# Performance work log

Measured on AMD Instinct MI355X. Metric: run time of the kernel, lower is better.

## Reference

```python
import jax, jax.numpy as jnp
import numpy as np
from math import sqrt

B, L, S, H, E, D = 2, 2048, 2048, 8, 64, 64


def setup_inputs() -> dict:
    key = jax.random.key(0)
    kq, kk, kv, kb = jax.random.split(key, 4)
    queries = jax.random.normal(kq, (B, L, H, E), dtype=jnp.float32)
    keys = jax.random.normal(kk, (B, S, H, E), dtype=jnp.float32)
    values = jax.random.normal(kv, (B, S, H, D), dtype=jnp.float32)
    # TriangularCausalMask: True above the diagonal (positions to mask)
    causal = jnp.triu(jnp.ones((L, S), dtype=bool), k=1)
    attn_mask = jnp.broadcast_to(causal[None, None], (B, 1, L, S))
    attn_bias = jax.random.normal(kb, (B, L, S, H), dtype=jnp.float32) * 0.1
    return {"queries": queries, "keys": keys, "values": values,
            "attn_mask": attn_mask, "attn_bias": attn_bias}


def reference(queries, keys, values, attn_mask, attn_bias):
    scale = 1.0 / sqrt(E)
    # scores: [B, H, L, S]
    scores = jnp.einsum('blhe,bshe->bhls', queries, keys)
    scores = jnp.where(attn_mask, -jnp.inf, scores)
    bias = jnp.transpose(attn_bias, (0, 3, 1, 2))  # [B,H,L,S]
    A = jax.nn.softmax(scores * scale + bias, axis=-1)  # dropout = identity (eval)
    V = jnp.einsum('bhls,bshd->blhd', A, values)
    return V
```

## Files before the change

### kernel.cpp

```cpp
#include <hip/hip_runtime.h>
#include <stdint.h>

#define Bb 2
#define Ll 2048
#define Ss 2048
#define Hh 8
#define Ee 64
#define Dd 64

#define LOG2E 1.4426950408889634f
#define QSCALE (0.125f * LOG2E)
#define NEG_BIG (-1e30f)
#define QT_ELEMS 2097152

typedef short bf16x8 __attribute__((ext_vector_type(8)));
typedef short bf16x4 __attribute__((ext_vector_type(4)));
typedef float f32x4  __attribute__((ext_vector_type(4)));

__device__ __forceinline__ short f2bf(float f) {
  uint32_t u = __float_as_uint(f);
  u += 0x7fffu + ((u >> 16) & 1u);
  return (short)(u >> 16);
}
__device__ __forceinline__ float bf2f(short s) {
  return __uint_as_float(((uint32_t)(unsigned short)s) << 16);
}
__device__ __forceinline__ f32x4 mfma_pv(bf16x4 a, bf16x4 b, f32x4 c) {
#if __has_builtin(__builtin_amdgcn_mfma_f32_16x16x16_bf16)
  return __builtin_amdgcn_mfma_f32_16x16x16_bf16(a, b, c, 0, 0, 0);
#else
  return __builtin_amdgcn_mfma_f32_16x16x16bf16_1k(a, b, c, 0, 0, 0);
#endif
}

#define BLOCK_SYNC() do {                                   \
    asm volatile("s_waitcnt lgkmcnt(0)" ::: "memory");      \
    __builtin_amdgcn_s_barrier();                           \
    asm volatile("" ::: "memory");                          \
  } while (0)

__global__ __launch_bounds__(256)
void prep_qkv(const float* __restrict__ Q, const float* __restrict__ K,
              const float* __restrict__ V, short* __restrict__ Qt,
              short* __restrict__ Kt, short* __restrict__ Vt)
{
  const int blk = blockIdx.x;
  const int tid = threadIdx.x;
  if (blk < 1024) {
    const int c = tid & 15;
    #pragma unroll
    for (int pass = 0; pass < 4; ++pass) {
      const int rowg = blk * 64 + pass * 16 + (tid >> 4);
      const int tensor = rowg >> 15;
      const int r2 = rowg & 32767;
      const float* src = (tensor ? K : Q) + (size_t)r2 * 64 + c * 4;
      const float4 v = *(const float4*)(src);
      const int b = r2 >> 14, l = (r2 >> 3) & 2047, hh = r2 & 7;
      const float sc = tensor ? 1.0f : QSCALE;
      bf16x4 o;
      o[0] = f2bf(v.x * sc); o[1] = f2bf(v.y * sc);
      o[2] = f2bf(v.z * sc); o[3] = f2bf(v.w * sc);
      short* dst = (tensor ? Kt : Qt) + ((size_t)((b * 8 + hh) * 2048 + l)) * 64 + c * 4;
      *reinterpret_cast<bf16x4*>(dst) = o;
    }
  } else {
    const int vb = blk - 1024;
    const int plane = vb >> 5;
    const int b = plane >> 3, hh = plane & 7;
    const int sc = (vb & 31) * 64;
    const int w = tid >> 6, d = tid & 63;
    const int sbase = sc + w * 16;
    const float* src = V + (((size_t)b * Ss + sbase) * Hh + hh) * Dd + d;
    float vals[16];
    #pragma unroll
    for (int i = 0; i < 16; ++i) vals[i] = src[(size_t)i * (Hh * Dd)];
    bf16x8 o0, o1;
    #pragma unroll
    for (int i = 0; i < 8; ++i) { o0[i] = f2bf(vals[i]); o1[i] = f2bf(vals[i + 8]); }
    short* dst = Vt + ((size_t)(plane * 64 + d)) * 2048 + sbase;
    *reinterpret_cast<bf16x8*>(dst)     = o0;
    *reinterpret_cast<bf16x8*>(dst + 8) = o1;
  }
}

__global__ __launch_bounds__(256, 1)
void fattn6(const short* __restrict__ Qt, const short* __restrict__ Kt,
            const short* __restrict__ Vt, const float* __restrict__ Bias,
            float* __restrict__ Out)
{
  __shared__ short Vs[2][4][64][72];
  __shared__ short Bs[2][4][4][16][16];

  const int tid  = threadIdx.x;
  const int wv   = tid >> 6;
  const int lane = tid & 63;
  const int g    = lane >> 4;
  const int n    = lane & 15;

  const int rid    = blockIdx.x;
  const int xcd    = rid & 7;
  const int b      = xcd >> 2;
  const int hhalf  = (xcd >> 1) & 1;
  const int z      = xcd & 1;
  const int pairid = (rid >> 3) * 2 + z;
  const int h      = hhalf * 4 + wv;
  const int p      = b * 8 + h;

  const int sl = tid >> 4;
  const int sq = tid & 15;
  const int srcb = (lane & 48) | ((lane >> 2) & 12);

  const short* vglob = Vt + ((size_t)((b * 8 + hhalf * 4) * 64) + (tid >> 3)) * 2048
                          + (tid & 7) * 8;
  short* vlds = &Vs[0][0][tid >> 3][(tid & 7) * 8];

#define ISSUE_V(VN, soff) do {                                              \
    _Pragma("unroll")                                                       \
    for (int k_ = 0; k_ < 8; ++k_)                                          \
      VN[k_] = *reinterpret_cast<const bf16x8*>(                            \
          vglob + (size_t)(k_ >> 1) * (64 * 2048)                           \
                + (size_t)(k_ & 1) * (32 * 2048) + (soff));                 \
  } while (0)

#define WRITE_V(buf, VN) do {                                               \
    _Pragma("unroll")                                                       \
    for (int k_ = 0; k_ < 8; ++k_)                                          \
      *reinterpret_cast<bf16x8*>(vlds + (size_t)(buf) * (4 * 64 * 72)       \
          + (k_ >> 1) * (64 * 72) + (k_ & 1) * (32 * 72)) = VN[k_];         \
  } while (0)

  for (int job = 0; job < 2; ++job) {
    const int lg = job ? pairid : (127 - pairid);
    const int l0 = lg * 16;
    const int ntiles = (lg >> 2) + 1;
    const int lq = l0 + n;

    const short* qp = Qt + ((size_t)(p * 2048 + l0 + n)) * 64 + g * 8;
    const bf16x8 qf0 = *reinterpret_cast<const bf16x8*>(qp);
    const bf16x8 qf1 = *reinterpret_cast<const bf16x8*>(qp + 32);

    const short* kbase = Kt + ((size_t)(p * 2048 + n)) * 64 + g * 8;
    const float* gb = Bias + (((size_t)(b * Ll + l0 + sl)) * Ss + sq) * Hh + hhalf * 4;

    f32x4 acc[4];
    #pragma unroll
    for (int dt = 0; dt < 4; ++dt) { f32x4 zz = {0.f,0.f,0.f,0.f}; acc[dt] = zz; }
    float m = NEG_BIG, lsum = 0.f;

    bf16x8 kA[4][2], kB[4][2];
    float4 gB0, gB1, gB2, gB3;

#define ISSUE_K(KN, soff) do {                                              \
      const short* kp_ = kbase + (size_t)(soff) * 64;                       \
      _Pragma("unroll")                                                     \
      for (int st_ = 0; st_ < 4; ++st_) {                                   \
        KN[st_][0] = *reinterpret_cast<const bf16x8*>(kp_ + st_ * 16 * 64); \
        KN[st_][1] = *reinterpret_cast<const bf16x8*>(kp_ + st_ * 16 * 64 + 32); \
      }                                                                     \
    } while (0)

#define ISSUE_BIAS(G0, G1, G2, G3, soff) do {                               \
      const float* gp_ = gb + (size_t)(soff) * Hh;                          \
      G0 = *(const float4*)(gp_);                                           \
      G1 = *(const float4*)(gp_ + (size_t)16 * Hh);                         \
      G2 = *(const float4*)(gp_ + (size_t)32 * Hh);                         \
      G3 = *(const float4*)(gp_ + (size_t)48 * Hh);                         \
    } while (0)

#define WRITE_BIAS(buf, G0, G1, G2, G3) do {                                \
      short* w0_ = &Bs[buf][0][0][sl][sq];                                  \
      short* w1_ = &Bs[buf][0][1][sl][sq];                                  \
      short* w2_ = &Bs[buf][0][2][sl][sq];                                  \
      short* w3_ = &Bs[buf][0][3][sl][sq];                                  \
      w0_[0]=f2bf(G0.x*LOG2E); w0_[1024]=f2bf(G0.y*LOG2E); w0_[2048]=f2bf(G0.z*LOG2E); w0_[3072]=f2bf(G0.w*LOG2E); \
      w1_[0]=f2bf(G1.x*LOG2E); w1_[1024]=f2bf(G1.y*LOG2E); w1_[2048]=f2bf(G1.z*LOG2E); w1_[3072]=f2bf(G1.w*LOG2E); \
      w2_[0]=f2bf(G2.x*LOG2E); w2_[1024]=f2bf(G2.y*LOG2E); w2_[2048]=f2bf(G2.z*LOG2E); w2_[3072]=f2bf(G2.w*LOG2E); \
      w3_[0]=f2bf(G3.x*LOG2E); w3_[1024]=f2bf(G3.y*LOG2E); w3_[2048]=f2bf(G3.z*LOG2E); w3_[3072]=f2bf(G3.w*LOG2E); \
    } while (0)

    {
      float4 a0, a1, a2, a3;
      ISSUE_BIAS(a0, a1, a2, a3, 0);
      ISSUE_BIAS(gB0, gB1, gB2, gB3, 64);
      ISSUE_K(kA, 0);
      bf16x8 v0[8];
      ISSUE_V(v0, 0);
      WRITE_BIAS(0, a0, a1, a2, a3);
      WRITE_V(0, v0);
    }
    BLOCK_SYNC();

#define TILE(KC, KN, t) do {                                                \
      const int s0_ = (t) * 64;                                             \
      const int cb_ = (t) & 1, nb_ = cb_ ^ 1;                               \
      const bool more1_ = ((t) + 1 < ntiles);                               \
      const bool more2_ = ((t) + 2 < ntiles);                               \
                 \
      if (more1_) ISSUE_K(KN, s0_ + 64);                                    \
      bf16x8 vN_[8];                                                        \
      if (more1_) ISSUE_V(vN_, s0_ + 64);                                   \
                                                    \
      f32x4 sacc_[4];                                                       \
      _Pragma("unroll")                                                     \
      for (int st_ = 0; st_ < 4; ++st_) {                                   \
        const bf16x4 bb_ = *reinterpret_cast<const bf16x4*>(&Bs[cb_][wv][st_][n][4 * g]); \
        f32x4 zz_ = {0.f, 0.f, 0.f, 0.f};                                   \
        f32x4 sv_ = __builtin_amdgcn_mfma_f32_16x16x32_bf16(KC[st_][0], qf0, zz_, 0, 0, 0); \
        sv_ = __builtin_amdgcn_mfma_f32_16x16x32_bf16(KC[st_][1], qf1, sv_, 0, 0, 0); \
        const int sb_ = s0_ + st_ * 16 + 4 * g;                             \
        _Pragma("unroll")                                                   \
        for (int r_ = 0; r_ < 4; ++r_)                                      \
          sacc_[st_][r_] = (sb_ + r_ <= lq) ? (sv_[r_] + bf2f(bb_[r_])) : NEG_BIG; \
      }                                                                     \
                                            \
      float tm_ = NEG_BIG;                                                  \
      _Pragma("unroll")                                                     \
      for (int st_ = 0; st_ < 4; ++st_)                                     \
        _Pragma("unroll")                                                   \
        for (int r_ = 0; r_ < 4; ++r_) tm_ = fmaxf(tm_, sacc_[st_][r_]);    \
      tm_ = fmaxf(tm_, __shfl_xor(tm_, 16));                                \
      tm_ = fmaxf(tm_, __shfl_xor(tm_, 32));                                \
      if (__any(tm_ - m > 8.f)) {                                           \
        const float mn_ = fmaxf(m, tm_);                                    \
        const float corr_ = exp2f(m - mn_);                                 \
        m = mn_; lsum *= corr_;                                             \
        const float c0_ = __shfl(corr_, srcb);                              \
        const float c1_ = __shfl(corr_, srcb + 1);                          \
        const float c2_ = __shfl(corr_, srcb + 2);                          \
        const float c3_ = __shfl(corr_, srcb + 3);                          \
        _Pragma("unroll")                                                   \
        for (int dt_ = 0; dt_ < 4; ++dt_) {                                 \
          acc[dt_][0] *= c0_; acc[dt_][1] *= c1_;                           \
          acc[dt_][2] *= c2_; acc[dt_][3] *= c3_;                           \
        }                                                                   \
      }                                                                     \
      bf16x4 pa_[4];                                                        \
      float ps_ = 0.f;                                                      \
      _Pragma("unroll")                                                     \
      for (int st_ = 0; st_ < 4; ++st_) {                                   \
        _Pragma("unroll")                                                   \
        for (int r_ = 0; r_ < 4; ++r_) {                                    \
          const float pe_ = exp2f(sacc_[st_][r_] - m);                      \
          ps_ += pe_;                                                       \
          pa_[st_][r_] = f2bf(pe_);                                         \
        }                                                                   \
      }                                                                     \
      ps_ += __shfl_xor(ps_, 16);                                           \
      ps_ += __shfl_xor(ps_, 32);                                           \
      lsum += ps_;                                                          \
                   \
      _Pragma("unroll")                                                     \
      for (int st_ = 0; st_ < 4; ++st_) {                                   \
        _Pragma("unroll")                                                   \
        for (int dt_ = 0; dt_ < 4; ++dt_) {                                 \
          const bf16x4 vb_ = *reinterpret_cast<const bf16x4*>(              \
              &Vs[cb_][wv][dt_ * 16 + n][st_ * 16 + 4 * g]);                \
          acc[dt_] = mfma_pv(pa_[st_], vb_, acc[dt_]);                      \
        }                                                                   \
      }                                                                     \
                                  \
      if (more1_) {                                                         \
        WRITE_V(nb_, vN_);                                                  \
        WRITE_BIAS(nb_, gB0, gB1, gB2, gB3);                                \
      }                                                                     \
      if (more2_) ISSUE_BIAS(gB0, gB1, gB2, gB3, s0_ + 128);                \
      BLOCK_SYNC();                                                         \
    } while (0)

    int t = 0;
    for (;;) {
      TILE(kA, kB, t); if (++t == ntiles) break;
      TILE(kB, kA, t); if (++t == ntiles) break;
    }

    const float i0 = 1.0f / __shfl(lsum, srcb);
    const float i1 = 1.0f / __shfl(lsum, srcb + 1);
    const float i2 = 1.0f / __shfl(lsum, srcb + 2);
    const float i3 = 1.0f / __shfl(lsum, srcb + 3);
    float* ob = Out + ((size_t)((b * Ll + l0 + 4 * g) * Hh + h)) * Dd + n;
    #pragma unroll
    for (int dt = 0; dt < 4; ++dt) {
      ob[0 * Hh * Dd + dt * 16] = acc[dt][0] * i0;
      ob[1 * Hh * Dd + dt * 16] = acc[dt][1] * i1;
      ob[2 * Hh * Dd + dt * 16] = acc[dt][2] * i2;
      ob[3 * Hh * Dd + dt * 16] = acc[dt][3] * i3;
    }

#undef TILE
#undef WRITE_BIAS
#undef ISSUE_BIAS
#undef ISSUE_K
  }
#undef WRITE_V
#undef ISSUE_V
}

extern "C" void kernel_launch(void* const* d_in, const int* in_sizes, int n_in,
                              void* d_out, int out_size, void* d_ws, size_t ws_size,
                              hipStream_t stream) {
  const float* Q    = (const float*)d_in[0];
  const float* K    = (const float*)d_in[1];
  const float* V    = (const float*)d_in[2];
  const float* Bias = (const float*)d_in[4];
  float* Out = (float*)d_out;

  short* wsp = (short*)d_ws;
  short* Qt = wsp;
  short* Kt = wsp + QT_ELEMS;
  short* Vt = wsp + 2 * (size_t)QT_ELEMS;

  prep_qkv<<<dim3(1536), dim3(256), 0, stream>>>(Q, K, V, Qt, Kt, Vt);
  fattn6<<<dim3(256), dim3(256), 0, stream>>>(Qt, Kt, Vt, Bias, Out);
}
```

Before: 94.14 us.

## Split each key tile across two wave groups with split-softmax merge

Doubles the block to 512 threads so two groups of four waves each process half of every 64-key tile, with per-group running max and sum. At the end the two partial accumulators are merged through shared memory using max and exp rescaling before the output is written. The goal is more waves in flight per CU to hide latency on this memory- and latency-bound causal attention. In exchange it adds extra shared memory, extra block barriers, and a final merge step. The masked score value also changes to a more negative sentinel.

After: 83.03 us. 11.8% less time.

```diff
diff --git a/kernel.cpp b/kernel.cpp
--- a/kernel.cpp
+++ b/kernel.cpp
@@ -10,7 +10,8 @@
 
 #define LOG2E 1.4426950408889634f
 #define QSCALE (0.125f * LOG2E)
-#define NEG_BIG (-1e30f)
+#define NEG_BIG  (-1e30f)
+#define NEG_MASK (-3.0e38f)
 #define QT_ELEMS 2097152
 
 typedef short bf16x8 __attribute__((ext_vector_type(8)));
@@ -83,16 +84,20 @@
   }
 }
 
-__global__ __launch_bounds__(256, 1)
-void fattn6(const short* __restrict__ Qt, const short* __restrict__ Kt,
+__global__ __launch_bounds__(512, 2)
+void fattn8(const short* __restrict__ Qt, const short* __restrict__ Kt,
             const short* __restrict__ Vt, const float* __restrict__ Bias,
             float* __restrict__ Out)
 {
   __shared__ short Vs[2][4][64][72];
   __shared__ short Bs[2][4][4][16][16];
+  __shared__ float Os[4][16][68];
+  __shared__ float mb[2][4][16];
+  __shared__ float lb[2][4][16];
 
   const int tid  = threadIdx.x;
-  const int wv   = tid >> 6;
+  const int sh   = tid >> 8;
+  const int wv   = (tid >> 6) & 3;
   const int lane = tid & 63;
   const int g    = lane >> 4;
   const int n    = lane & 15;
@@ -105,28 +110,27 @@
   const int pairid = (rid >> 3) * 2 + z;
   const int h      = hhalf * 4 + wv;
   const int p      = b * 8 + h;
-
-  const int sl = tid >> 4;
-  const int sq = tid & 15;
+  const int p0     = b * 8 + hhalf * 4;
+
+  const int vch = tid & 7;
+  const int vr  = (tid >> 3) & 63;
+  const short* vglob = Vt + ((size_t)(p0 * 64 + vr)) * 2048 + vch * 8;
+
+  const int sl  = tid >> 5;
+  const int sq2 = tid & 31;
   const int srcb = (lane & 48) | ((lane >> 2) & 12);
-
-  const short* vglob = Vt + ((size_t)((b * 8 + hhalf * 4) * 64) + (tid >> 3)) * 2048
-                          + (tid & 7) * 8;
-  short* vlds = &Vs[0][0][tid >> 3][(tid & 7) * 8];
 
 #define ISSUE_V(VN, soff) do {                                              \
     _Pragma("unroll")                                                       \
-    for (int k_ = 0; k_ < 8; ++k_)                                          \
+    for (int k_ = 0; k_ < 4; ++k_)                                          \
       VN[k_] = *reinterpret_cast<const bf16x8*>(                            \
-          vglob + (size_t)(k_ >> 1) * (64 * 2048)                           \
-                + (size_t)(k_ & 1) * (32 * 2048) + (soff));                 \
+          vglob + (size_t)k_ * (64 * 2048) + (soff));                       \
   } while (0)
 
 #define WRITE_V(buf, VN) do {                                               \
     _Pragma("unroll")                                                       \
-    for (int k_ = 0; k_ < 8; ++k_)                                          \
-      *reinterpret_cast<bf16x8*>(vlds + (size_t)(buf) * (4 * 64 * 72)       \
-          + (k_ >> 1) * (64 * 72) + (k_ & 1) * (32 * 72)) = VN[k_];         \
+    for (int k_ = 0; k_ < 4; ++k_)                                          \
+      *reinterpret_cast<bf16x8*>(&Vs[buf][k_][vr][vch * 8]) = VN[k_];       \
   } while (0)
 
   for (int job = 0; job < 2; ++job) {
@@ -139,53 +143,52 @@
     const bf16x8 qf0 = *reinterpret_cast<const bf16x8*>(qp);
     const bf16x8 qf1 = *reinterpret_cast<const bf16x8*>(qp + 32);
 
-    const short* kbase = Kt + ((size_t)(p * 2048 + n)) * 64 + g * 8;
-    const float* gb = Bias + (((size_t)(b * Ll + l0 + sl)) * Ss + sq) * Hh + hhalf * 4;
+    const short* kbase = Kt + ((size_t)(p * 2048 + sh * 32 + n)) * 64 + g * 8;
+    const float* gb = Bias + (((size_t)(b * Ll + l0 + sl)) * Ss + sq2) * Hh + hhalf * 4;
 
     f32x4 acc[4];
     #pragma unroll
     for (int dt = 0; dt < 4; ++dt) { f32x4 zz = {0.f,0.f,0.f,0.f}; acc[dt] = zz; }
     float m = NEG_BIG, lsum = 0.f;
 
-    bf16x8 kA[4][2], kB[4][2];
-    float4 gB0, gB1, gB2, gB3;
+    bf16x8 kA[2][2], kB[2][2];
+    float4 gB0, gB1;
 
 #define ISSUE_K(KN, soff) do {                                              \
       const short* kp_ = kbase + (size_t)(soff) * 64;                       \
       _Pragma("unroll")                                                     \
-      for (int st_ = 0; st_ < 4; ++st_) {                                   \
+      for (int st_ = 0; st_ < 2; ++st_) {                                   \
         KN[st_][0] = *reinterpret_cast<const bf16x8*>(kp_ + st_ * 16 * 64); \
         KN[st_][1] = *reinterpret_cast<const bf16x8*>(kp_ + st_ * 16 * 64 + 32); \
       }                                                                     \
     } while (0)
 
-#define ISSUE_BIAS(G0, G1, G2, G3, soff) do {                               \
+#define ISSUE_BIAS(G0, G1, soff) do {                                       \
       const float* gp_ = gb + (size_t)(soff) * Hh;                          \
       G0 = *(const float4*)(gp_);                                           \
-      G1 = *(const float4*)(gp_ + (size_t)16 * Hh);                         \
-      G2 = *(const float4*)(gp_ + (size_t)32 * Hh);                         \
-      G3 = *(const float4*)(gp_ + (size_t)48 * Hh);                         \
+      G1 = *(const float4*)(gp_ + (size_t)32 * Hh);                         \
     } while (0)
 
-#define WRITE_BIAS(buf, G0, G1, G2, G3) do {                                \
-      short* w0_ = &Bs[buf][0][0][sl][sq];                                  \
-      short* w1_ = &Bs[buf][0][1][sl][sq];                                  \
-      short* w2_ = &Bs[buf][0][2][sl][sq];                                  \
-      short* w3_ = &Bs[buf][0][3][sl][sq];                                  \
-      w0_[0]=f2bf(G0.x*LOG2E); w0_[1024]=f2bf(G0.y*LOG2E); w0_[2048]=f2bf(G0.z*LOG2E); w0_[3072]=f2bf(G0.w*LOG2E); \
-      w1_[0]=f2bf(G1.x*LOG2E); w1_[1024]=f2bf(G1.y*LOG2E); w1_[2048]=f2bf(G1.z*LOG2E); w1_[3072]=f2bf(G1.w*LOG2E); \
-      w2_[0]=f2bf(G2.x*LOG2E); w2_[1024]=f2bf(G2.y*LOG2E); w2_[2048]=f2bf(G2.z*LOG2E); w2_[3072]=f2bf(G2.w*LOG2E); \
-      w3_[0]=f2bf(G3.x*LOG2E); w3_[1024]=f2bf(G3.y*LOG2E); w3_[2048]=f2bf(G3.z*LOG2E); w3_[3072]=f2bf(G3.w*LOG2E); \
+#define WRITE_BIAS(buf, G0, G1) do {                                        \
+      const int st0_ = sq2 >> 4, s16_ = sq2 & 15;                           \
+      Bs[buf][0][st0_][sl][s16_]     = f2bf(G0.x * LOG2E);                  \
+      Bs[buf][1][st0_][sl][s16_]     = f2bf(G0.y * LOG2E);                  \
+      Bs[buf][2][st0_][sl][s16_]     = f2bf(G0.z * LOG2E);                  \
+      Bs[buf][3][st0_][sl][s16_]     = f2bf(G0.w * LOG2E);                  \
+      Bs[buf][0][st0_ + 2][sl][s16_] = f2bf(G1.x * LOG2E);                  \
+      Bs[buf][1][st0_ + 2][sl][s16_] = f2bf(G1.y * LOG2E);                  \
+      Bs[buf][2][st0_ + 2][sl][s16_] = f2bf(G1.z * LOG2E);                  \
+      Bs[buf][3][st0_ + 2][sl][s16_] = f2bf(G1.w * LOG2E);                  \
     } while (0)
 
     {
-      float4 a0, a1, a2, a3;
-      ISSUE_BIAS(a0, a1, a2, a3, 0);
-      ISSUE_BIAS(gB0, gB1, gB2, gB3, 64);
+      float4 a0, a1;
+      ISSUE_BIAS(a0, a1, 0);
+      ISSUE_BIAS(gB0, gB1, 64);
       ISSUE_K(kA, 0);
-      bf16x8 v0[8];
+      bf16x8 v0[4];
       ISSUE_V(v0, 0);
-      WRITE_BIAS(0, a0, a1, a2, a3);
+      WRITE_BIAS(0, a0, a1);
       WRITE_V(0, v0);
     }
     BLOCK_SYNC();
@@ -195,29 +198,29 @@
       const int cb_ = (t) & 1, nb_ = cb_ ^ 1;                               \
       const bool more1_ = ((t) + 1 < ntiles);                               \
       const bool more2_ = ((t) + 2 < ntiles);                               \
-                 \
       if (more1_) ISSUE_K(KN, s0_ + 64);                                    \
-      bf16x8 vN_[8];                                                        \
+      bf16x8 vN_[4];                                                        \
       if (more1_) ISSUE_V(vN_, s0_ + 64);                                   \
-                                                    \
-      f32x4 sacc_[4];                                                       \
-      _Pragma("unroll")                                                     \
-      for (int st_ = 0; st_ < 4; ++st_) {                                   \
-        const bf16x4 bb_ = *reinterpret_cast<const bf16x4*>(&Bs[cb_][wv][st_][n][4 * g]); \
+                            \
+      f32x4 sacc_[2];                                                       \
+      _Pragma("unroll")                                                     \
+      for (int stl_ = 0; stl_ < 2; ++stl_) {                                \
+        const int stg_ = 2 * sh + stl_;                                     \
+        const bf16x4 bb_ = *reinterpret_cast<const bf16x4*>(&Bs[cb_][wv][stg_][n][4 * g]); \
         f32x4 zz_ = {0.f, 0.f, 0.f, 0.f};                                   \
-        f32x4 sv_ = __builtin_amdgcn_mfma_f32_16x16x32_bf16(KC[st_][0], qf0, zz_, 0, 0, 0); \
-        sv_ = __builtin_amdgcn_mfma_f32_16x16x32_bf16(KC[st_][1], qf1, sv_, 0, 0, 0); \
-        const int sb_ = s0_ + st_ * 16 + 4 * g;                             \
+        f32x4 sv_ = __builtin_amdgcn_mfma_f32_16x16x32_bf16(KC[stl_][0], qf0, zz_, 0, 0, 0); \
+        sv_ = __builtin_amdgcn_mfma_f32_16x16x32_bf16(KC[stl_][1], qf1, sv_, 0, 0, 0); \
+        const int sb_ = s0_ + stg_ * 16 + 4 * g;                            \
         _Pragma("unroll")                                                   \
         for (int r_ = 0; r_ < 4; ++r_)                                      \
-          sacc_[st_][r_] = (sb_ + r_ <= lq) ? (sv_[r_] + bf2f(bb_[r_])) : NEG_BIG; \
-      }                                                                     \
-                                            \
-      float tm_ = NEG_BIG;                                                  \
-      _Pragma("unroll")                                                     \
-      for (int st_ = 0; st_ < 4; ++st_)                                     \
-        _Pragma("unroll")                                                   \
-        for (int r_ = 0; r_ < 4; ++r_) tm_ = fmaxf(tm_, sacc_[st_][r_]);    \
+          sacc_[stl_][r_] = (sb_ + r_ <= lq) ? (sv_[r_] + bf2f(bb_[r_])) : NEG_MASK; \
+      }                                                                     \
+                      \
+      float tm_ = NEG_MASK;                                                 \
+      _Pragma("unroll")                                                     \
+      for (int stl_ = 0; stl_ < 2; ++stl_)                                  \
+        _Pragma("unroll")                                                   \
+        for (int r_ = 0; r_ < 4; ++r_) tm_ = fmaxf(tm_, sacc_[stl_][r_]);   \
       tm_ = fmaxf(tm_, __shfl_xor(tm_, 16));                                \
       tm_ = fmaxf(tm_, __shfl_xor(tm_, 32));                                \
       if (__any(tm_ - m > 8.f)) {                                           \
@@ -234,36 +237,37 @@
           acc[dt_][2] *= c2_; acc[dt_][3] *= c3_;                           \
         }                                                                   \
       }                                                                     \
-      bf16x4 pa_[4];                                                        \
+      bf16x4 pa_[2];                                                        \
       float ps_ = 0.f;                                                      \
       _Pragma("unroll")                                                     \
-      for (int st_ = 0; st_ < 4; ++st_) {                                   \
+      for (int stl_ = 0; stl_ < 2; ++stl_) {                                \
         _Pragma("unroll")                                                   \
         for (int r_ = 0; r_ < 4; ++r_) {                                    \
-          const float pe_ = exp2f(sacc_[st_][r_] - m);                      \
+          const float pe_ = exp2f(sacc_[stl_][r_] - m);                     \
           ps_ += pe_;                                                       \
-          pa_[st_][r_] = f2bf(pe_);                                         \
+          pa_[stl_][r_] = f2bf(pe_);                                        \
         }                                                                   \
       }                                                                     \
       ps_ += __shfl_xor(ps_, 16);                                           \
       ps_ += __shfl_xor(ps_, 32);                                           \
       lsum += ps_;                                                          \
-                   \
-      _Pragma("unroll")                                                     \
-      for (int st_ = 0; st_ < 4; ++st_) {                                   \
+                                             \
+      _Pragma("unroll")                                                     \
+      for (int stl_ = 0; stl_ < 2; ++stl_) {                                \
+        const int stg_ = 2 * sh + stl_;                                     \
         _Pragma("unroll")                                                   \
         for (int dt_ = 0; dt_ < 4; ++dt_) {                                 \
           const bf16x4 vb_ = *reinterpret_cast<const bf16x4*>(              \
-              &Vs[cb_][wv][dt_ * 16 + n][st_ * 16 + 4 * g]);                \
-          acc[dt_] = mfma_pv(pa_[st_], vb_, acc[dt_]);                      \
+              &Vs[cb_][wv][dt_ * 16 + n][stg_ * 16 + 4 * g]);               \
+          acc[dt_] = mfma_pv(pa_[stl_], vb_, acc[dt_]);                     \
         }                                                                   \
       }                                                                     \
                                   \
       if (more1_) {                                                         \
         WRITE_V(nb_, vN_);                                                  \
-        WRITE_BIAS(nb_, gB0, gB1, gB2, gB3);                                \
-      }                                                                     \
-      if (more2_) ISSUE_BIAS(gB0, gB1, gB2, gB3, s0_ + 128);                \
+        WRITE_BIAS(nb_, gB0, gB1);                                          \
+      }                                                                     \
+      if (more2_) ISSUE_BIAS(gB0, gB1, s0_ + 128);                          \
       BLOCK_SYNC();                                                         \
     } while (0)
 
@@ -273,18 +277,36 @@
       TILE(kB, kA, t); if (++t == ntiles) break;
     }
 
-    const float i0 = 1.0f / __shfl(lsum, srcb);
-    const float i1 = 1.0f / __shfl(lsum, srcb + 1);
-    const float i2 = 1.0f / __shfl(lsum, srcb + 2);
-    const float i3 = 1.0f / __shfl(lsum, srcb + 3);
-    float* ob = Out + ((size_t)((b * Ll + l0 + 4 * g) * Hh + h)) * Dd + n;
-    #pragma unroll
-    for (int dt = 0; dt < 4; ++dt) {
-      ob[0 * Hh * Dd + dt * 16] = acc[dt][0] * i0;
-      ob[1 * Hh * Dd + dt * 16] = acc[dt][1] * i1;
-      ob[2 * Hh * Dd + dt * 16] = acc[dt][2] * i2;
-      ob[3 * Hh * Dd + dt * 16] = acc[dt][3] * i3;
-    }
+    if (lane < 16) { mb[sh][wv][lane] = m; lb[sh][wv][lane] = lsum; }
+    BLOCK_SYNC();
+    if (sh == 0) {
+      #pragma unroll
+      for (int r = 0; r < 4; ++r) {
+        const int row = 4 * g + r;
+        const float M  = fmaxf(mb[0][wv][row], mb[1][wv][row]);
+        const float sc = exp2f(mb[0][wv][row] - M);
+        #pragma unroll
+        for (int dt = 0; dt < 4; ++dt)
+          Os[wv][row][dt * 16 + n] = acc[dt][r] * sc;
+      }
+    }
+    BLOCK_SYNC();
+    if (sh == 1) {
+      #pragma unroll
+      for (int r = 0; r < 4; ++r) {
+        const int row = 4 * g + r;
+        const float M   = fmaxf(mb[0][wv][row], mb[1][wv][row]);
+        const float sc1 = exp2f(mb[1][wv][row] - M);
+        const float L   = lb[0][wv][row] * exp2f(mb[0][wv][row] - M)
+                        + lb[1][wv][row] * sc1;
+        const float inv = 1.0f / L;
+        float* op = Out + (((size_t)(b * Ll + l0 + row)) * Hh + h) * Dd + n;
+        #pragma unroll
+        for (int dt = 0; dt < 4; ++dt)
+          op[dt * 16] = (Os[wv][row][dt * 16 + n] + acc[dt][r] * sc1) * inv;
+      }
+    }
+    BLOCK_SYNC();
 
 #undef TILE
 #undef WRITE_BIAS
@@ -310,5 +332,5 @@
   short* Vt = wsp + 2 * (size_t)QT_ELEMS;
 
   prep_qkv<<<dim3(1536), dim3(256), 0, stream>>>(Q, K, V, Qt, Kt, Vt);
-  fattn6<<<dim3(256), dim3(256), 0, stream>>>(Qt, Kt, Vt, Bias, Out);
-}
+  fattn8<<<dim3(256), dim3(512), 0, stream>>>(Qt, Kt, Vt, Bias, Out);
+}
```
